# Kernel optimization log

Measured on AMD Instinct MI355X. Metric: run time of the kernel, lower is better.

## Reference

```python
import jax, jax.numpy as jnp
import numpy as np

N_NODES = 100000
N_EDGES = 3200000
IN_FEATS = 512
HIDDEN = 16
NUM_CLASSES = 40


def setup_inputs() -> dict:
    key = jax.random.key(0)
    k1, k2, k3, k4, k5, k6 = jax.random.split(key, 6)
    x = jax.random.normal(k1, (N_NODES, IN_FEATS), dtype=jnp.float32)
    edge_index = jax.random.randint(k2, (2, N_EDGES), 0, N_NODES, dtype=jnp.int64)
    # Glorot-ish init for GCN weights
    W1 = jax.random.normal(k3, (IN_FEATS, HIDDEN), dtype=jnp.float32) / np.sqrt(IN_FEATS)
    b1 = jnp.zeros((HIDDEN,), dtype=jnp.float32)
    W2 = jax.random.normal(k4, (HIDDEN, NUM_CLASSES), dtype=jnp.float32) / np.sqrt(HIDDEN)
    b2 = jnp.zeros((NUM_CLASSES,), dtype=jnp.float32)
    return {"x": x, "edge_index": edge_index, "W1": W1, "b1": b1, "W2": W2, "b2": b2}


def _gcn_norm(edge_index, num_nodes):
    # Add self-loops (PyG GCNConv default), then symmetric normalization
    loops = jnp.arange(num_nodes, dtype=edge_index.dtype)
    src = jnp.concatenate([edge_index[0], loops])
    dst = jnp.concatenate([edge_index[1], loops])
    deg = jax.ops.segment_sum(jnp.ones_like(dst, dtype=jnp.float32), dst,
                              num_segments=num_nodes)
    dinv = jnp.where(deg > 0, jax.lax.rsqrt(deg), 0.0)
    norm = dinv[src] * dinv[dst]  # [E + N]
    return src, dst, norm


def _gcn_conv(x, W, b, src, dst, norm, num_nodes):
    h = x @ W                                   # transform first: [N, d_out]
    msg = h[src] * norm[:, None]                # gather + scale: [E+N, d_out]
    agg = jax.ops.segment_sum(msg, dst, num_segments=num_nodes)
    return agg + b


def reference(x, edge_index, W1, b1, W2, b2):
    num_nodes = x.shape[0]
    src, dst, norm = _gcn_norm(edge_index, num_nodes)
    h = _gcn_conv(x, W1, b1, src, dst, norm, num_nodes)
    h = jax.nn.relu(h)
    # F.dropout(training=self.training): eval mode -> identity (deterministic reference)
    h = _gcn_conv(h, W2, b2, src, dst, norm, num_nodes)
    return jax.nn.log_softmax(h, axis=1)
```

## Files before the change

kernel.cpp:

```cpp
#include <hip/hip_runtime.h>
#include <hip/hip_bf16.h>
#include <math.h>

#define N_NODES 100000
#define N_EDGES 3200000
#define IN_F    512
#define HID     16
#define NCLS    40
#define NB      512
#define NPB     196
#define CAPW    8192
#define NBLK    1024
#define EPB     3125

typedef unsigned short ushort_t;

__device__ __forceinline__ float bf16_to_f32(ushort_t u) {
    unsigned int b = ((unsigned int)u) << 16;
    return __uint_as_float(b);
}
__device__ __forceinline__ ushort_t f32_to_bf16(float f) {
    __hip_bfloat16 h = __float2bfloat16(f);
    return *(ushort_t*)&h;
}

__device__ __forceinline__ int load_edge(const void* ei, int is64, int idx) {
    if (is64) return (int)((const long long*)ei)[idx];
    return ((const int*)ei)[idx];
}

__global__ __launch_bounds__(256) void kPre(const int* __restrict__ ei,
                                            int* __restrict__ flag,
                                            int* __restrict__ gcur) {
    int i = blockIdx.x * 256 + threadIdx.x;
    if (i < NB) gcur[i] = i * CAPW;
    if (blockIdx.x == 0) {
        __shared__ int s_nz;
        if (threadIdx.x == 0) s_nz = 0;
        __syncthreads();
        int nz = 0;
        for (int k = threadIdx.x; k < 1024; k += 256)
            if (ei[2 * k + 1] != 0) nz = 1;
        if (nz) atomicOr(&s_nz, 1);
        __syncthreads();
        if (threadIdx.x == 0) flag[0] = s_nz ? 0 : 1;
    }
}

__global__ __launch_bounds__(256) void kB(const void* __restrict__ ei,
                                          const int* __restrict__ flag,
                                          int* __restrict__ gcur,
                                          int* __restrict__ binned) {
    __shared__ int hist[NB];
    __shared__ int base[NB];
    for (int i = threadIdx.x; i < NB; i += 256) hist[i] = 0;
    __syncthreads();
    int is64 = flag[0];
    int off0 = blockIdx.x * EPB;
    for (int i = threadIdx.x; i < EPB; i += 256) {
        int d = load_edge(ei, is64, N_EDGES + off0 + i);
        atomicAdd(&hist[d / NPB], 1);
    }
    __syncthreads();
    for (int i = threadIdx.x; i < NB; i += 256) {
        int c = hist[i];
        base[i] = c ? atomicAdd(&gcur[i], c) : 0;
        hist[i] = 0;
    }
    __syncthreads();
    for (int i = threadIdx.x; i < EPB; i += 256) {
        int s = load_edge(ei, is64, off0 + i);
        int d = load_edge(ei, is64, N_EDGES + off0 + i);
        int b = d / NPB;
        int o = atomicAdd(&hist[b], 1);
        binned[base[b] + o] = (s << 8) | (d - b * NPB);
    }
}

__global__ __launch_bounds__(256) void kSort(const int* __restrict__ gcur,
                                             int* __restrict__ binned,
                                             int* __restrict__ nstart,
                                             int* __restrict__ bend,
                                             float* __restrict__ dinv) {
    __shared__ int elist[CAPW];
    __shared__ int ih[NPB];
    __shared__ int lscan[NPB + 1];
    int b = blockIdx.x, tid = threadIdx.x;
    int beg = b * CAPW;
    int cnt = gcur[b] - beg;
    if (cnt > CAPW) cnt = CAPW;
    if (cnt < 0) cnt = 0;
    if (tid < NPB) ih[tid] = 0;
    __syncthreads();
    for (int k = tid; k < cnt; k += 256) {
        int p = binned[beg + k];
        elist[k] = p;
        atomicAdd(&ih[p & 255], 1);
    }
    __syncthreads();
    if (tid == 0) {
        int run = 0;
        for (int i = 0; i < NPB; ++i) { lscan[i] = run; run += ih[i]; }
        lscan[NPB] = run;
        bend[b] = beg + run;
    }
    __syncthreads();
    if (tid < NPB) {
        int n = b * NPB + tid;
        if (n < N_NODES) dinv[n] = rsqrtf((float)(ih[tid] + 1));
        nstart[n] = beg + lscan[tid];
        ih[tid] = lscan[tid];
    }
    __syncthreads();
    for (int k = tid; k < cnt; k += 256) {
        int p = elist[k];
        int pos = atomicAdd(&ih[p & 255], 1);
        binned[beg + pos] = p >> 8;
    }
}

__global__ __launch_bounds__(128) void k_gemm1(const float* __restrict__ x,
                                               const float* __restrict__ W1,
                                               const float* __restrict__ dinv,
                                               ushort_t* __restrict__ hsb) {
    __shared__ float Ws[IN_F * HID];
    for (int i = threadIdx.x; i < IN_F * HID; i += 128) Ws[i] = W1[i];
    __syncthreads();
    int n = blockIdx.x * 128 + threadIdx.x;
    if (n >= N_NODES) return;
    float acc[HID];
#pragma unroll
    for (int j = 0; j < HID; ++j) acc[j] = 0.0f;
    const float4* xr = (const float4*)(x + (size_t)n * IN_F);
    for (int k4 = 0; k4 < IN_F / 4; ++k4) {
        float4 xv = xr[k4];
        int kb = k4 * 4;
#pragma unroll
        for (int i = 0; i < 4; ++i) {
            float xs = (&xv.x)[i];
            const float4* wr = (const float4*)(Ws + (kb + i) * HID);
#pragma unroll
            for (int j4 = 0; j4 < 4; ++j4) {
                float4 w = wr[j4];
                acc[j4 * 4 + 0] += xs * w.x;
                acc[j4 * 4 + 1] += xs * w.y;
                acc[j4 * 4 + 2] += xs * w.z;
                acc[j4 * 4 + 3] += xs * w.w;
            }
        }
    }
    float di = dinv[n];
    ushort_t* hn = hsb + (size_t)n * HID;
#pragma unroll
    for (int j = 0; j < HID; ++j) hn[j] = f32_to_bf16(acc[j] * di);
}

__global__ __launch_bounds__(256) void kAgg1(const int* __restrict__ nstart,
                                             const int* __restrict__ bend,
                                             const int* __restrict__ sorted,
                                             const ushort_t* __restrict__ hsb,
                                             const float* __restrict__ dinv,
                                             const float* __restrict__ b1,
                                             ushort_t* __restrict__ h1sb) {
    int tid = threadIdx.x;
    int g = tid >> 4, lane = tid & 15;
    int n = blockIdx.x * 16 + g;
    int b = n / NPB, il = n - b * NPB;
    int beg = nstart[n];
    int end = (il == NPB - 1) ? bend[b] : nstart[n + 1];
    float acc = 0.0f;
    int k = beg;
    for (; k + 4 <= end; k += 4) {
        int s0 = sorted[k + 0], s1 = sorted[k + 1];
        int s2 = sorted[k + 2], s3 = sorted[k + 3];
        float v0 = bf16_to_f32(hsb[(size_t)s0 * HID + lane]);
        float v1 = bf16_to_f32(hsb[(size_t)s1 * HID + lane]);
        float v2 = bf16_to_f32(hsb[(size_t)s2 * HID + lane]);
        float v3 = bf16_to_f32(hsb[(size_t)s3 * HID + lane]);
        acc += (v0 + v1) + (v2 + v3);
    }
    for (; k < end; ++k)
        acc += bf16_to_f32(hsb[(size_t)sorted[k] * HID + lane]);
    float di = dinv[n];
    float self = bf16_to_f32(hsb[(size_t)n * HID + lane]);
    float v = di * (acc + self) + b1[lane];
    h1sb[(size_t)n * HID + lane] = f32_to_bf16(fmaxf(v, 0.0f) * di);
}

__global__ __launch_bounds__(256) void kAggOut(const int* __restrict__ nstart,
                                               const int* __restrict__ bend,
                                               const int* __restrict__ sorted,
                                               const ushort_t* __restrict__ h1sb,
                                               const float* __restrict__ dinv,
                                               const float* __restrict__ W2,
                                               const float* __restrict__ b2,
                                               float* __restrict__ out) {
    __shared__ float a2[16][HID + 1];
    __shared__ float Ws[HID * NCLS];
    __shared__ float bs[NCLS];
    int tid = threadIdx.x;
    for (int i = tid; i < HID * NCLS; i += 256) Ws[i] = W2[i];
    for (int i = tid; i < NCLS; i += 256) bs[i] = b2[i];

    int g = tid >> 4, lane = tid & 15;
    int n = blockIdx.x * 16 + g;
    int b = n / NPB, il = n - b * NPB;
    int beg = nstart[n];
    int end = (il == NPB - 1) ? bend[b] : nstart[n + 1];
    float acc = 0.0f;
    int k = beg;
    for (; k + 4 <= end; k += 4) {
        int s0 = sorted[k + 0], s1 = sorted[k + 1];
        int s2 = sorted[k + 2], s3 = sorted[k + 3];
        float v0 = bf16_to_f32(h1sb[(size_t)s0 * HID + lane]);
        float v1 = bf16_to_f32(h1sb[(size_t)s1 * HID + lane]);
        float v2 = bf16_to_f32(h1sb[(size_t)s2 * HID + lane]);
        float v3 = bf16_to_f32(h1sb[(size_t)s3 * HID + lane]);
        acc += (v0 + v1) + (v2 + v3);
    }
    for (; k < end; ++k)
        acc += bf16_to_f32(h1sb[(size_t)sorted[k] * HID + lane]);
    float di = dinv[n];
    float self = bf16_to_f32(h1sb[(size_t)n * HID + lane]);
    a2[g][lane] = di * (acc + self);
    __syncthreads();

    int v = g, cidx = lane;
    float av[HID];
#pragma unroll
    for (int j = 0; j < HID; ++j) av[j] = a2[v][j];
    float l0 = bs[cidx], l1 = bs[cidx + 16];
    float l2 = (cidx < 8) ? bs[cidx + 32] : -1e30f;
#pragma unroll
    for (int j = 0; j < HID; ++j) {
        const float* wr = Ws + j * NCLS;
        l0 += av[j] * wr[cidx];
        l1 += av[j] * wr[cidx + 16];
        if (cidx < 8) l2 += av[j] * wr[cidx + 32];
    }
    float m = fmaxf(l0, fmaxf(l1, l2));
#pragma unroll
    for (int off = 8; off >= 1; off >>= 1)
        m = fmaxf(m, __shfl_xor(m, off, 16));
    float e = expf(l0 - m) + expf(l1 - m) + ((cidx < 8) ? expf(l2 - m) : 0.0f);
#pragma unroll
    for (int off = 8; off >= 1; off >>= 1)
        e += __shfl_xor(e, off, 16);
    float lse = m + logf(e);
    int nn = blockIdx.x * 16 + v;
    float* on = out + (size_t)nn * NCLS;
    on[cidx] = l0 - lse;
    on[cidx + 16] = l1 - lse;
    if (cidx < 8) on[cidx + 32] = l2 - lse;
}

extern "C" void kernel_launch(void* const* d_in, const int* in_sizes, int n_in,
                              void* d_out, int out_size, void* d_ws, size_t ws_size,
                              hipStream_t stream) {
    const float* x  = (const float*)d_in[0];
    const void*  ei = d_in[1];
    const float* W1 = (const float*)d_in[2];
    const float* b1 = (const float*)d_in[3];
    const float* W2 = (const float*)d_in[4];
    const float* b2 = (const float*)d_in[5];
    float* out = (float*)d_out;

    int*      iws    = (int*)d_ws;
    float*    fws    = (float*)d_ws;
    int*      gcur   = iws;
    int*      bend   = iws + 2048;
    int*      flag   = iws + 4096;
    float*    dinv   = fws + 8192;
    int*      nstart = iws + 108192;
    ushort_t* hsb    = (ushort_t*)(iws + 212992);
    ushort_t* h1sb   = (ushort_t*)(iws + 1012992);
    int*      binned = iws + 1812992;

    const int B = 256;

    kPre<<<(NB + B - 1) / B, B, 0, stream>>>((const int*)ei, flag, gcur);
    kB<<<NBLK, B, 0, stream>>>(ei, flag, gcur, binned);
    kSort<<<NB, B, 0, stream>>>(gcur, binned, nstart, bend, dinv);
    k_gemm1<<<(N_NODES + 127) / 128, 128, 0, stream>>>(x, W1, dinv, hsb);
    kAgg1<<<N_NODES / 16, B, 0, stream>>>(nstart, bend, binned, hsb, dinv, b1, h1sb);
    kAggOut<<<N_NODES / 16, B, 0, stream>>>(nstart, bend, binned, h1sb, dinv, W2, b2, out);
}
```

Baseline: 233.6 us.

## Fuse GCN pipeline into one cooperative kernel with block-resident sorted edges

```diff
diff --git a/kernel.cpp b/kernel.cpp
--- a/kernel.cpp
+++ b/kernel.cpp
@@ -1,15 +1,18 @@
 #include <hip/hip_runtime.h>
 #include <hip/hip_bf16.h>
+#include <hip/hip_cooperative_groups.h>
 #include <math.h>
+
+namespace cg = cooperative_groups;
 
 #define N_NODES 100000
 #define N_EDGES 3200000
 #define IN_F    512
 #define HID     16
 #define NCLS    40
-#define NB      512
-#define NPB     196
-#define CAPW    8192
+#define NB      1024
+#define NPB     98
+#define CAPW    4096
 #define NBLK    1024
 #define EPB     3125
 
@@ -27,6 +30,224 @@
 __device__ __forceinline__ int load_edge(const void* ei, int is64, int idx) {
     if (is64) return (int)((const long long*)ei)[idx];
     return ((const int*)ei)[idx];
+}
+
+__global__ __launch_bounds__(256, 4) void kCoop(const float* __restrict__ x,
+                                                const void* __restrict__ ei,
+                                                const float* __restrict__ W1,
+                                                const float* __restrict__ b1,
+                                                const float* __restrict__ W2,
+                                                const float* __restrict__ b2,
+                                                float* __restrict__ out,
+                                                int* __restrict__ gcur,
+                                                int* __restrict__ flag,
+                                                float* __restrict__ dinv,
+                                                ushort_t* __restrict__ hsb,
+                                                ushort_t* __restrict__ h1sb,
+                                                int* __restrict__ binned) {
+    __shared__ __align__(16) int bufA[CAPW];
+    __shared__ __align__(16) int bufB[CAPW];
+    __shared__ int ih[NPB];
+    __shared__ int lscan[NPB + 1];
+    __shared__ float sdinv[NPB];
+    __shared__ int s_nz;
+
+    cg::grid_group grid = cg::this_grid();
+    int tid = threadIdx.x, blk = blockIdx.x;
+
+    if (tid == 0) gcur[blk] = blk * CAPW;
+    if (blk == 0) {
+        if (tid == 0) s_nz = 0;
+        __syncthreads();
+        int nz = 0;
+        for (int k = tid; k < 1024; k += 256)
+            if (((const int*)ei)[2 * k + 1] != 0) nz = 1;
+        if (nz) atomicOr(&s_nz, 1);
+        __syncthreads();
+        if (tid == 0) flag[0] = s_nz ? 0 : 1;
+    }
+    grid.sync();
+    int is64 = flag[0];
+
+    {
+        int* hist = bufA;
+        int* base = bufA + NB;
+        for (int i = tid; i < NB; i += 256) hist[i] = 0;
+        __syncthreads();
+        int off0 = blk * EPB;
+        for (int i = tid; i < EPB; i += 256) {
+            int d = load_edge(ei, is64, N_EDGES + off0 + i);
+            atomicAdd(&hist[d / NPB], 1);
+        }
+        __syncthreads();
+        for (int i = tid; i < NB; i += 256) {
+            int c = hist[i];
+            base[i] = c ? atomicAdd(&gcur[i], c) : 0;
+            hist[i] = 0;
+        }
+        __syncthreads();
+        for (int i = tid; i < EPB; i += 256) {
+            int s = load_edge(ei, is64, off0 + i);
+            int d = load_edge(ei, is64, N_EDGES + off0 + i);
+            int b = d / NPB;
+            int o = atomicAdd(&hist[b], 1);
+            binned[base[b] + o] = (s << 7) | (d - b * NPB);
+        }
+    }
+    grid.sync();
+
+    {
+        int beg = blk * CAPW;
+        int cnt = gcur[blk] - beg;
+        if (cnt > CAPW) cnt = CAPW;
+        if (cnt < 0) cnt = 0;
+        if (tid < NPB) ih[tid] = 0;
+        __syncthreads();
+        for (int k = tid; k < cnt; k += 256) {
+            int p = binned[beg + k];
+            bufA[k] = p;
+            atomicAdd(&ih[p & 127], 1);
+        }
+        __syncthreads();
+        if (tid == 0) {
+            int run = 0;
+            for (int i = 0; i < NPB; ++i) { lscan[i] = run; run += ih[i]; }
+            lscan[NPB] = run;
+        }
+        __syncthreads();
+        if (tid < NPB) {
+            int n = blk * NPB + tid;
+            float di = rsqrtf((float)(ih[tid] + 1));
+            sdinv[tid] = di;
+            if (n < N_NODES) dinv[n] = di;
+            ih[tid] = lscan[tid];
+        }
+        __syncthreads();
+        for (int k = tid; k < cnt; k += 256) {
+            int p = bufA[k];
+            int pos = atomicAdd(&ih[p & 127], 1);
+            bufB[pos] = p >> 7;
+        }
+    }
+    grid.sync();
+
+    {
+        int n = blk * 256 + tid;
+        if (n < N_NODES) {
+            float acc[HID];
+#pragma unroll
+            for (int j = 0; j < HID; ++j) acc[j] = 0.0f;
+            const float4* xr = (const float4*)(x + (size_t)n * IN_F);
+            for (int k4 = 0; k4 < IN_F / 4; ++k4) {
+                float4 xv = xr[k4];
+                int kb = k4 * 4;
+#pragma unroll
+                for (int i = 0; i < 4; ++i) {
+                    float xs = (&xv.x)[i];
+                    const float* wr = W1 + (kb + i) * HID;
+#pragma unroll
+                    for (int j = 0; j < HID; ++j) acc[j] += xs * wr[j];
+                }
+            }
+            float di = dinv[n];
+            ushort_t* hn = hsb + (size_t)n * HID;
+#pragma unroll
+            for (int j = 0; j < HID; ++j) hn[j] = f32_to_bf16(acc[j] * di);
+        }
+    }
+    grid.sync();
+
+    {
+        int g = tid >> 4, lane = tid & 15;
+        for (int il = g; il < NPB; il += 16) {
+            int n = blk * NPB + il;
+            if (n < N_NODES) {
+                int bl = lscan[il], el = lscan[il + 1];
+                float acc = 0.0f;
+                int k = bl;
+                for (; k + 4 <= el; k += 4) {
+                    int s0 = bufB[k + 0], s1 = bufB[k + 1];
+                    int s2 = bufB[k + 2], s3 = bufB[k + 3];
+                    float v0 = bf16_to_f32(hsb[(size_t)s0 * HID + lane]);
+                    float v1 = bf16_to_f32(hsb[(size_t)s1 * HID + lane]);
+                    float v2 = bf16_to_f32(hsb[(size_t)s2 * HID + lane]);
+                    float v3 = bf16_to_f32(hsb[(size_t)s3 * HID + lane]);
+                    acc += (v0 + v1) + (v2 + v3);
+                }
+                for (; k < el; ++k)
+                    acc += bf16_to_f32(hsb[(size_t)bufB[k] * HID + lane]);
+                float di = sdinv[il];
+                float self = bf16_to_f32(hsb[(size_t)n * HID + lane]);
+                float v = di * (acc + self) + b1[lane];
+                h1sb[(size_t)n * HID + lane] = f32_to_bf16(fmaxf(v, 0.0f) * di);
+            }
+        }
+    }
+    grid.sync();
+
+    {
+        float* w2s = (float*)bufA;
+        float* bsc = w2s + HID * NCLS;
+        float* a2  = bsc + NCLS;
+        for (int i = tid; i < HID * NCLS; i += 256) w2s[i] = W2[i];
+        for (int i = tid; i < NCLS; i += 256) bsc[i] = b2[i];
+        __syncthreads();
+        int g = tid >> 4, lane = tid & 15;
+        const int NBATCH = (NPB + 15) / 16;
+        for (int batch = 0; batch < NBATCH; ++batch) {
+            int il = batch * 16 + g;
+            int n = blk * NPB + il;
+            bool valid = (il < NPB) && (n < N_NODES);
+            float a = 0.0f;
+            if (valid) {
+                int bl = lscan[il], el = lscan[il + 1];
+                float acc = 0.0f;
+                int k = bl;
+                for (; k + 4 <= el; k += 4) {
+                    int s0 = bufB[k + 0], s1 = bufB[k + 1];
+                    int s2 = bufB[k + 2], s3 = bufB[k + 3];
+                    float v0 = bf16_to_f32(h1sb[(size_t)s0 * HID + lane]);
+                    float v1 = bf16_to_f32(h1sb[(size_t)s1 * HID + lane]);
+                    float v2 = bf16_to_f32(h1sb[(size_t)s2 * HID + lane]);
+                    float v3 = bf16_to_f32(h1sb[(size_t)s3 * HID + lane]);
+                    acc += (v0 + v1) + (v2 + v3);
+                }
+                for (; k < el; ++k)
+                    acc += bf16_to_f32(h1sb[(size_t)bufB[k] * HID + lane]);
+                float self = bf16_to_f32(h1sb[(size_t)n * HID + lane]);
+                a = sdinv[il] * (acc + self);
+            }
+            a2[g * 17 + lane] = a;
+            __syncthreads();
+            if (valid) {
+                float l0 = bsc[lane], l1 = bsc[lane + 16];
+                float l2 = (lane < 8) ? bsc[lane + 32] : -1e30f;
+#pragma unroll
+                for (int j = 0; j < HID; ++j) {
+                    float av = a2[g * 17 + j];
+                    const float* wr = w2s + j * NCLS;
+                    l0 += av * wr[lane];
+                    l1 += av * wr[lane + 16];
+                    if (lane < 8) l2 += av * wr[lane + 32];
+                }
+                float m = fmaxf(l0, fmaxf(l1, l2));
+#pragma unroll
+                for (int off = 8; off >= 1; off >>= 1)
+                    m = fmaxf(m, __shfl_xor(m, off, 16));
+                float e = expf(l0 - m) + expf(l1 - m) +
+                          ((lane < 8) ? expf(l2 - m) : 0.0f);
+#pragma unroll
+                for (int off = 8; off >= 1; off >>= 1)
+                    e += __shfl_xor(e, off, 16);
+                float lse = m + logf(e);
+                float* on = out + (size_t)n * NCLS;
+                on[lane] = l0 - lse;
+                on[lane + 16] = l1 - lse;
+                if (lane < 8) on[lane + 32] = l2 - lse;
+            }
+            __syncthreads();
+        }
+    }
 }
 
 __global__ __launch_bounds__(256) void kPre(const int* __restrict__ ei,
@@ -73,7 +294,7 @@
         int d = load_edge(ei, is64, N_EDGES + off0 + i);
         int b = d / NPB;
         int o = atomicAdd(&hist[b], 1);
-        binned[base[b] + o] = (s << 8) | (d - b * NPB);
+        binned[base[b] + o] = (s << 7) | (d - b * NPB);
     }
 }
 
@@ -95,7 +316,7 @@
     for (int k = tid; k < cnt; k += 256) {
         int p = binned[beg + k];
         elist[k] = p;
-        atomicAdd(&ih[p & 255], 1);
+        atomicAdd(&ih[p & 127], 1);
     }
     __syncthreads();
     if (tid == 0) {
@@ -114,8 +335,8 @@
     __syncthreads();
     for (int k = tid; k < cnt; k += 256) {
         int p = elist[k];
-        int pos = atomicAdd(&ih[p & 255], 1);
-        binned[beg + pos] = p >> 8;
+        int pos = atomicAdd(&ih[p & 127], 1);
+        binned[beg + pos] = p >> 7;
     }
 }
 
@@ -201,7 +422,6 @@
     int tid = threadIdx.x;
     for (int i = tid; i < HID * NCLS; i += 256) Ws[i] = W2[i];
     for (int i = tid; i < NCLS; i += 256) bs[i] = b2[i];
-
     int g = tid >> 4, lane = tid & 15;
     int n = blockIdx.x * 16 + g;
     int b = n / NPB, il = n - b * NPB;
@@ -224,34 +444,29 @@
     float self = bf16_to_f32(h1sb[(size_t)n * HID + lane]);
     a2[g][lane] = di * (acc + self);
     __syncthreads();
-
-    int v = g, cidx = lane;
-    float av[HID];
-#pragma unroll
-    for (int j = 0; j < HID; ++j) av[j] = a2[v][j];
-    float l0 = bs[cidx], l1 = bs[cidx + 16];
-    float l2 = (cidx < 8) ? bs[cidx + 32] : -1e30f;
+    float l0 = bs[lane], l1 = bs[lane + 16];
+    float l2 = (lane < 8) ? bs[lane + 32] : -1e30f;
 #pragma unroll
     for (int j = 0; j < HID; ++j) {
+        float av = a2[g][j];
         const float* wr = Ws + j * NCLS;
-        l0 += av[j] * wr[cidx];
-        l1 += av[j] * wr[cidx + 16];
-        if (cidx < 8) l2 += av[j] * wr[cidx + 32];
+        l0 += av * wr[lane];
+        l1 += av * wr[lane + 16];
+        if (lane < 8) l2 += av * wr[lane + 32];
     }
     float m = fmaxf(l0, fmaxf(l1, l2));
 #pragma unroll
     for (int off = 8; off >= 1; off >>= 1)
         m = fmaxf(m, __shfl_xor(m, off, 16));
-    float e = expf(l0 - m) + expf(l1 - m) + ((cidx < 8) ? expf(l2 - m) : 0.0f);
+    float e = expf(l0 - m) + expf(l1 - m) + ((lane < 8) ? expf(l2 - m) : 0.0f);
 #pragma unroll
     for (int off = 8; off >= 1; off >>= 1)
         e += __shfl_xor(e, off, 16);
     float lse = m + logf(e);
-    int nn = blockIdx.x * 16 + v;
-    float* on = out + (size_t)nn * NCLS;
-    on[cidx] = l0 - lse;
-    on[cidx + 16] = l1 - lse;
-    if (cidx < 8) on[cidx + 32] = l2 - lse;
+    float* on = out + (size_t)n * NCLS;
+    on[lane] = l0 - lse;
+    on[lane + 16] = l1 - lse;
+    if (lane < 8) on[lane + 32] = l2 - lse;
 }
 
 extern "C" void kernel_launch(void* const* d_in, const int* in_sizes, int n_in,
@@ -268,16 +483,24 @@
     int*      iws    = (int*)d_ws;
     float*    fws    = (float*)d_ws;
     int*      gcur   = iws;
-    int*      bend   = iws + 2048;
-    int*      flag   = iws + 4096;
-    float*    dinv   = fws + 8192;
-    int*      nstart = iws + 108192;
+    int*      bend   = iws + 1024;
+    int*      flag   = iws + 2048;
+    int*      nstart = iws + 8192;
+    float*    dinv   = fws + 112640;
     ushort_t* hsb    = (ushort_t*)(iws + 212992);
-    ushort_t* h1sb   = (ushort_t*)(iws + 1012992);
-    int*      binned = iws + 1812992;
+    ushort_t* h1sb   = (ushort_t*)(iws + 1015808);
+    int*      binned = iws + 1818624;
+
+    void* args[] = {(void*)&x, (void*)&ei, (void*)&W1, (void*)&b1,
+                    (void*)&W2, (void*)&b2, (void*)&out,
+                    (void*)&gcur, (void*)&flag, (void*)&dinv,
+                    (void*)&hsb, (void*)&h1sb, (void*)&binned};
+    hipError_t err = hipLaunchCooperativeKernel((const void*)kCoop,
+                                                dim3(NB), dim3(256),
+                                                args, 0, stream);
+    if (err == hipSuccess) return;
 
     const int B = 256;
-
     kPre<<<(NB + B - 1) / B, B, 0, stream>>>((const int*)ei, flag, gcur);
     kB<<<NBLK, B, 0, stream>>>(ei, flag, gcur, binned);
     kSort<<<NB, B, 0, stream>>>(gcur, binned, nstart, bend, dinv);
```

New measurement: 832.2 us. 3.56x slower.
